# Kernel tuning notes

Hardware: AMD Instinct MI355X
Metric: run time of the kernel (lower is better)

The kernel has to match this reference:

```python
import jax, jax.numpy as jnp
import numpy as np

B, N, C = 2048, 4096, 1024
UNITS, RANK = 4096, 512


def _orth(key, shape):
    a = jax.random.normal(key, shape, dtype=jnp.float32)
    q, r = jnp.linalg.qr(a if shape[0] >= shape[1] else a.T)
    q = q * jnp.sign(jnp.diagonal(r))[None, :]
    return q if shape[0] >= shape[1] else q.T


def setup_inputs() -> dict:
    key = jax.random.key(0)
    k1, k2, k3, k4, k5, k6 = jax.random.split(key, 6)
    inputs = jax.random.normal(k1, (B, N), dtype=jnp.float32)
    context = jax.random.normal(k2, (B, C), dtype=jnp.float32)
    U = _orth(k3, (N, RANK))
    V = _orth(k4, (UNITS, RANK))
    W = _orth(k5, (C, RANK))
    # SingularValueInitializer stand-in: positive values scaled like glorot singular values
    S = jnp.abs(jax.random.normal(k6, (RANK,), dtype=jnp.float32)) * jnp.sqrt(2.0 / (N + UNITS))
    bias = jnp.zeros((UNITS,), dtype=jnp.float32)
    return {"inputs": inputs, "context": context, "U": U, "S": S, "V": V, "W": W, "bias": bias}


def reference(inputs, context, U, S, V, W, bias):
    # s_b = S + context @ W  -> per-batch singular values [B, R]
    s = S[None, :] + context @ W
    # Original: kernel_b = U diag(s_b) V^T; out_b = x_b @ kernel_b.
    # Associativity: out = ((x @ U) * s) @ V^T  -- identical math, no [B,N,M] intermediate.
    xu = inputs @ U                      # [B, R]
    out = (xu * s) @ V.T                 # [B, UNITS]
    out = out + bias[None, :]
    return jax.nn.relu(out)
```

## Files before the change

kernel.cpp:

```cpp
#include <hip/hip_runtime.h>
#include <hip/hip_bf16.h>

typedef __attribute__((ext_vector_type(8))) __bf16 bf16x8;
typedef __attribute__((ext_vector_type(4))) float f32x4;
typedef __attribute__((ext_vector_type(8))) unsigned short ushort8;
typedef __attribute__((ext_vector_type(4))) unsigned short ushort4v;

__device__ __forceinline__ unsigned short f2bf(float f) {
  unsigned u = __builtin_bit_cast(unsigned, f);
  u += 0x7FFFu + ((u >> 16) & 1u);
  return (unsigned short)(u >> 16);
}

__device__ __forceinline__ void gload_lds16(const void* g, void* l) {
  __builtin_amdgcn_global_load_lds(
      (const __attribute__((address_space(1))) void*)g,
      (__attribute__((address_space(3))) void*)l, 16, 0, 0);
}

__device__ __forceinline__ void barrier_fence() {
  __builtin_amdgcn_s_barrier();
  asm volatile("" ::: "memory");
}

template <int N>
__device__ __forceinline__ void waitvm() {
  if constexpr (N == 0)      asm volatile("s_waitcnt vmcnt(0)" ::: "memory");
  else if constexpr (N == 8) asm volatile("s_waitcnt vmcnt(8)" ::: "memory");
}

__global__ __launch_bounds__(256) void prep_kernel(
    const float* __restrict__ U, unsigned short* __restrict__ Ut,
    const float* __restrict__ W, unsigned short* __restrict__ Wt,
    const float* __restrict__ V, unsigned short* __restrict__ Vb) {
  __shared__ float tile[32][33];
  const int b = blockIdx.x;
  const int tid = threadIdx.x;
  if (b < 2560) {
    const float* src;
    unsigned short* dst;
    int rows, cols, bx, by;
    if (b < 2048) {
      src = U; dst = Ut; rows = 4096; cols = 512;
      bx = (b & 15) * 32; by = (b >> 4) * 32;
    } else {
      int bb = b - 2048;
      src = W; dst = Wt; rows = 1024; cols = 512;
      bx = (bb & 15) * 32; by = (bb >> 4) * 32;
    }
    const int tx = tid & 31, ty = tid >> 5;
    for (int i = ty; i < 32; i += 8)
      tile[i][tx] = src[(size_t)(by + i) * cols + bx + tx];
    __syncthreads();
    for (int i = ty; i < 32; i += 8)
      dst[(size_t)(bx + i) * rows + by + tx] = f2bf(tile[tx][i]);
  } else {
    const size_t i = (size_t)(b - 2560) * 256 + tid;
    const float4* s4 = reinterpret_cast<const float4*>(V) + 2 * i;
    float4 a = s4[0], c = s4[1];
    ushort8 o;
    o[0] = f2bf(a.x); o[1] = f2bf(a.y); o[2] = f2bf(a.z); o[3] = f2bf(a.w);
    o[4] = f2bf(c.x); o[5] = f2bf(c.y); o[6] = f2bf(c.z); o[7] = f2bf(c.w);
    *(reinterpret_cast<ushort8*>(Vb) + i) = o;
  }
}

template <int FM, int FN, int EPI, int DEPTH, bool COLMAP>
__device__ __forceinline__ void gemm_core(
    const unsigned short* __restrict__ A, const unsigned short* __restrict__ Bt,
    int N, int lda, int kchunk, const float* __restrict__ e0,
    float* __restrict__ outf, int nwg, int bid) {
  constexpr int BM = 32 * FM, BN = 32 * FN, BK = 64;
  constexpr int AI = FM, BI = FN;
  constexpr int ISS = AI + BI;
  __shared__ unsigned short lds[DEPTH][(BM + BN) * BK];

  const int tid = threadIdx.x;
  const int wid = tid >> 6;
  const int lane = tid & 63;
  const int wr = wid >> 1, wc = wid & 1;

  const int swz = (bid & 7) * (nwg >> 3) + (bid >> 3);
  const int nbn = N / BN;
  int brow, bcol;
  if constexpr (COLMAP) {
    const int nbm = nwg / nbn;
    brow = (swz % nbm) * BM;
    bcol = (swz / nbm) * BN;
  } else {
    brow = (swz / nbn) * BM;
    bcol = (swz % nbn) * BN;
  }

  f32x4 zero = {0.f, 0.f, 0.f, 0.f};
  f32x4 acc[FM][FN];
#pragma unroll
  for (int m = 0; m < FM; ++m)
#pragma unroll
    for (int n = 0; n < FN; ++n) acc[m][n] = zero;

  const int lr = lane >> 3;
  const int swzc = ((lane & 7) ^ lr) * 8;
  const unsigned short* Agh = A + (size_t)(brow + wid * (BM / 4) + lr) * lda + swzc;
  const unsigned short* Bgh = Bt + (size_t)(bcol + wid * (BN / 4) + lr) * lda + swzc;

  const int frow = lane & 15;
  const int fhi = lane >> 4;

  const int nsteps = kchunk / BK;

  auto stage = [&](int b, int kofs) {
    unsigned short* AsW = lds[b] + wid * (BM / 4) * 64;
#pragma unroll
    for (int i = 0; i < AI; ++i)
      gload_lds16(Agh + kofs + (size_t)(8 * i) * lda, AsW + i * 512);
    unsigned short* BsW = lds[b] + BM * BK + wid * (BN / 4) * 64;
#pragma unroll
    for (int i = 0; i < BI; ++i)
      gload_lds16(Bgh + kofs + (size_t)(8 * i) * lda, BsW + i * 512);
  };

  auto compute = [&](int cur) {
    const unsigned short* As = lds[cur];
    const unsigned short* Bs = lds[cur] + BM * BK;
#pragma unroll
    for (int ks = 0; ks < 2; ++ks) {
      bf16x8 af[FM], bg[FN];
#pragma unroll
      for (int m = 0; m < FM; ++m) {
        int row = wr * FM * 16 + m * 16 + frow;
        int pc = (ks * 4 + fhi) ^ (row & 7);
        af[m] = *reinterpret_cast<const bf16x8*>(As + row * 64 + pc * 8);
      }
#pragma unroll
      for (int n = 0; n < FN; ++n) {
        int row = wc * FN * 16 + n * 16 + frow;
        int pc = (ks * 4 + fhi) ^ (row & 7);
        bg[n] = *reinterpret_cast<const bf16x8*>(Bs + row * 64 + pc * 8);
      }
#pragma unroll
      for (int m = 0; m < FM; ++m)
#pragma unroll
        for (int n = 0; n < FN; ++n)
          acc[m][n] = __builtin_amdgcn_mfma_f32_16x16x32_bf16(af[m], bg[n],
                                                              acc[m][n], 0, 0, 0);
    }
  };

#pragma unroll
  for (int d = 0; d < DEPTH; ++d) stage(d, d * BK);

  int cur = 0;
  for (int t = 0; t < nsteps; ++t) {
    const int ahead = nsteps - 1 - t;
    if (ahead >= DEPTH - 1)
      waitvm<(DEPTH - 1) * ISS>();
    else
      waitvm<0>();
    barrier_fence();
    compute(cur);
    if (t + 1 < nsteps) {
      asm volatile("s_waitcnt lgkmcnt(0)" ::: "memory");
      barrier_fence();
      if (t + DEPTH < nsteps) stage(cur, (t + DEPTH) * BK);
    }
    cur = (cur + 1 == DEPTH) ? 0 : cur + 1;
  }

#pragma unroll
  for (int m = 0; m < FM; ++m) {
    int gr0 = brow + wr * FM * 16 + m * 16 + fhi * 4;
#pragma unroll
    for (int n = 0; n < FN; ++n) {
      int gc = bcol + wc * FN * 16 + n * 16 + frow;
#pragma unroll
      for (int j = 0; j < 4; ++j) {
        size_t idx = (size_t)(gr0 + j) * N + gc;
        float v = acc[m][n][j];
        if constexpr (EPI == 2) {
          v += e0[gc];
          outf[idx] = v > 0.f ? v : 0.f;
        } else {
          outf[idx] = v;
        }
      }
    }
  }
}

__device__ __forceinline__ void gemm_core_f32a(
    const float* __restrict__ A, const unsigned short* __restrict__ Bt,
    int lda, const float* __restrict__ e0,
    float* __restrict__ outf, int nwg, int bid) {
  constexpr int N = 512;
  constexpr int BM = 128, BN = 128, BK = 64;
  constexpr int kchunk = 1024;
  __shared__ unsigned short lds[2][(BM + BN) * BK];

  const int tid = threadIdx.x;
  const int wid = tid >> 6;
  const int lane = tid & 63;
  const int wr = wid >> 1, wc = wid & 1;

  const int swz = (bid & 7) * (nwg >> 3) + (bid >> 3);
  const int nbn = N / BN;
  const int brow = (swz / nbn) * BM;
  const int bcol = (swz % nbn) * BN;

  f32x4 zero = {0.f, 0.f, 0.f, 0.f};
  f32x4 acc[4][4];
#pragma unroll
  for (int m = 0; m < 4; ++m)
#pragma unroll
    for (int n = 0; n < 4; ++n) acc[m][n] = zero;

  const int lr = lane >> 3;
  const int lc = lane & 7;
  const int swzc = (lc ^ lr) * 8;
  const float* Agf = A + (size_t)(brow + wid * 32 + lr) * lda + swzc;
  const unsigned short* Bgh = Bt + (size_t)(bcol + wid * 32 + lr) * lda + swzc;

  const int frow = lane & 15;
  const int fhi = lane >> 4;

  const int nsteps = kchunk / BK;

  float4 areg[4][2];
  auto aload = [&](int kofs) {
#pragma unroll
    for (int i = 0; i < 4; ++i) {
      const float* s = Agf + kofs + (size_t)(8 * i) * lda;
      areg[i][0] = *reinterpret_cast<const float4*>(s);
      areg[i][1] = *reinterpret_cast<const float4*>(s + 4);
    }
  };
  auto awrite = [&](int b) {
    unsigned short* AsW = lds[b] + wid * 2048 + lane * 8;
#pragma unroll
    for (int i = 0; i < 4; ++i) {
      float4 x = areg[i][0], y = areg[i][1];
      ushort8 o;
      o[0] = f2bf(x.x); o[1] = f2bf(x.y); o[2] = f2bf(x.z); o[3] = f2bf(x.w);
      o[4] = f2bf(y.x); o[5] = f2bf(y.y); o[6] = f2bf(y.z); o[7] = f2bf(y.w);
      *reinterpret_cast<ushort8*>(AsW + i * 512) = o;
    }
  };
  auto bload = [&](int b, int kofs) {
    unsigned short* BsW = lds[b] + BM * BK + wid * 2048;
#pragma unroll
    for (int i = 0; i < 4; ++i)
      gload_lds16(Bgh + kofs + (size_t)(8 * i) * lda, BsW + i * 512);
  };

  auto compute = [&](int cur) {
    const unsigned short* As = lds[cur];
    const unsigned short* Bs = lds[cur] + BM * BK;
#pragma unroll
    for (int ks = 0; ks < 2; ++ks) {
      bf16x8 af[4], bg[4];
#pragma unroll
      for (int m = 0; m < 4; ++m) {
        int row = wr * 64 + m * 16 + frow;
        int pc = (ks * 4 + fhi) ^ (row & 7);
        af[m] = *reinterpret_cast<const bf16x8*>(As + row * 64 + pc * 8);
      }
#pragma unroll
      for (int n = 0; n < 4; ++n) {
        int row = wc * 64 + n * 16 + frow;
        int pc = (ks * 4 + fhi) ^ (row & 7);
        bg[n] = *reinterpret_cast<const bf16x8*>(Bs + row * 64 + pc * 8);
      }
#pragma unroll
      for (int m = 0; m < 4; ++m)
#pragma unroll
        for (int n = 0; n < 4; ++n)
          acc[m][n] = __builtin_amdgcn_mfma_f32_16x16x32_bf16(af[m], bg[n],
                                                              acc[m][n], 0, 0, 0);
    }
  };

  aload(0);
  bload(0, 0);
  waitvm<0>();
  awrite(0);
  aload(BK);
  asm volatile("s_waitcnt lgkmcnt(0)" ::: "memory");
  barrier_fence();

  for (int t = 0; t < nsteps; ++t) {
    const int cur = t & 1;
    if (t + 1 < nsteps) bload(cur ^ 1, (t + 1) * BK);
    compute(cur);
    if (t + 1 < nsteps) {
      waitvm<0>();
      awrite(cur ^ 1);
      if (t + 2 < nsteps) aload((t + 2) * BK);
      asm volatile("s_waitcnt lgkmcnt(0)" ::: "memory");
      barrier_fence();
    }
  }

#pragma unroll
  for (int m = 0; m < 4; ++m) {
    int gr0 = brow + wr * 64 + m * 16 + fhi * 4;
#pragma unroll
    for (int n = 0; n < 4; ++n) {
      int gc = bcol + wc * 64 + n * 16 + frow;
#pragma unroll
      for (int j = 0; j < 4; ++j) {
        float v = acc[m][n][j];
        if (e0) v += e0[gc];
        outf[(size_t)(gr0 + j) * N + gc] = v;
      }
    }
  }
}

__global__ __launch_bounds__(256) void gemm01_kernel(
    const float* __restrict__ inp, const unsigned short* __restrict__ Ut,
    const float* __restrict__ ctx, const unsigned short* __restrict__ Wt,
    const float* __restrict__ S, float* __restrict__ sbuf,
    float* __restrict__ p1) {
  const int bid = (int)blockIdx.x;
  constexpr size_t MN = (size_t)2048 * 512;
  const float* A;
  const unsigned short* Bt;
  int lda, nwg, lbid;
  const float* e0;
  float* outp;
  if (bid < 256) {
    const int split = bid >> 6;
    A = inp + (size_t)split * 1024;
    Bt = Ut + (size_t)split * 1024;
    lda = 4096; e0 = nullptr; outp = p1 + split * MN; nwg = 64; lbid = bid & 63;
  } else {
    A = ctx; Bt = Wt; lda = 1024; e0 = S; outp = sbuf; nwg = 64; lbid = bid - 256;
  }
  gemm_core_f32a(A, Bt, lda, e0, outp, nwg, lbid);
}

__global__ __launch_bounds__(256) void gemm2_kernel(
    const unsigned short* __restrict__ xus, const unsigned short* __restrict__ Vb,
    const float* __restrict__ bias, float* __restrict__ out) {
  gemm_core<4, 4, 2, 2, true>(xus, Vb, 4096, 512, 512, bias, out, 512,
                              (int)blockIdx.x);
}

__global__ void reduce_mul_kernel(const float* __restrict__ p1,
                                  const float* __restrict__ sbuf,
                                  unsigned short* __restrict__ xus, int MN) {
  int i = blockIdx.x * blockDim.x + threadIdx.x;
  size_t base = (size_t)i * 4;
  if (base >= (size_t)MN) return;
  float4 a = *reinterpret_cast<const float4*>(p1 + base);
  float4 b = *reinterpret_cast<const float4*>(p1 + (size_t)MN + base);
  float4 c = *reinterpret_cast<const float4*>(p1 + 2 * (size_t)MN + base);
  float4 d = *reinterpret_cast<const float4*>(p1 + 3 * (size_t)MN + base);
  float4 s = *reinterpret_cast<const float4*>(sbuf + base);
  float4 xu;
  xu.x = (a.x + b.x) + (c.x + d.x);
  xu.y = (a.y + b.y) + (c.y + d.y);
  xu.z = (a.z + b.z) + (c.z + d.z);
  xu.w = (a.w + b.w) + (c.w + d.w);
  ushort4v o;
  o[0] = f2bf(xu.x * s.x);
  o[1] = f2bf(xu.y * s.y);
  o[2] = f2bf(xu.z * s.z);
  o[3] = f2bf(xu.w * s.w);
  *reinterpret_cast<ushort4v*>(xus + base) = o;
}

extern "C" void kernel_launch(void* const* d_in, const int* in_sizes, int n_in,
                              void* d_out, int out_size, void* d_ws, size_t ws_size,
                              hipStream_t stream) {
  constexpr int Bm = 2048, Nn = 4096, Cc = 1024, UU = 4096, RR = 512;
  const float* inputs  = (const float*)d_in[0];
  const float* context = (const float*)d_in[1];
  const float* U       = (const float*)d_in[2];
  const float* S       = (const float*)d_in[3];
  const float* V       = (const float*)d_in[4];
  const float* W       = (const float*)d_in[5];
  const float* bias    = (const float*)d_in[6];
  float* out = (float*)d_out;

  char* p = (char*)d_ws;
  unsigned short* Ut   = (unsigned short*)p; p += (size_t)RR * Nn * 2;
  unsigned short* Wt   = (unsigned short*)p; p += (size_t)RR * Cc * 2;
  unsigned short* Vb   = (unsigned short*)p; p += (size_t)UU * RR * 2;
  float*          sbuf = (float*)p;          p += (size_t)Bm * RR * 4;
  float*          p1   = (float*)p;          p += (size_t)4 * Bm * RR * 4;
  unsigned short* xus  = (unsigned short*)p; p += (size_t)Bm * RR * 2;

  prep_kernel<<<3584, 256, 0, stream>>>(U, Ut, W, Wt, V, Vb);

  gemm01_kernel<<<320, 256, 0, stream>>>(inputs, Ut, context, Wt, S, sbuf, p1);

  reduce_mul_kernel<<<Bm * RR / 4 / 256, 256, 0, stream>>>(p1, sbuf, xus, Bm * RR);

  gemm2_kernel<<<512, 256, 0, stream>>>(xus, Vb, bias, out);
}
```

Measured before the change: 62.04 us.

## Store split-K partials in bf16 and split context GEMM to balance workgroups

The split-K partial sums of inputs@U and the context@W product are now written as bf16 instead of fp32, roughly halving partial-buffer traffic in both the GEMM epilogue and the reduce kernel. The context GEMM is also split into two K-chunks of 512, giving 384 workgroups all doing equal 512/1024-sized K work rather than 64 blocks doing a full 1024-K chunk. The S vector add moves into the reduce kernel, which now handles 8 elements per thread. Rounding the partials to bf16 before summation adds precision loss.

```diff
diff --git a/kernel.cpp b/kernel.cpp
--- a/kernel.cpp
+++ b/kernel.cpp
@@ -4,12 +4,15 @@
 typedef __attribute__((ext_vector_type(8))) __bf16 bf16x8;
 typedef __attribute__((ext_vector_type(4))) float f32x4;
 typedef __attribute__((ext_vector_type(8))) unsigned short ushort8;
-typedef __attribute__((ext_vector_type(4))) unsigned short ushort4v;
 
 __device__ __forceinline__ unsigned short f2bf(float f) {
   unsigned u = __builtin_bit_cast(unsigned, f);
   u += 0x7FFFu + ((u >> 16) & 1u);
   return (unsigned short)(u >> 16);
+}
+
+__device__ __forceinline__ float bf2f(unsigned short h) {
+  return __builtin_bit_cast(float, (unsigned)h << 16);
 }
 
 __device__ __forceinline__ void gload_lds16(const void* g, void* l) {
@@ -190,11 +193,9 @@
 
 __device__ __forceinline__ void gemm_core_f32a(
     const float* __restrict__ A, const unsigned short* __restrict__ Bt,
-    int lda, const float* __restrict__ e0,
-    float* __restrict__ outf, int nwg, int bid) {
+    int lda, int kchunk, unsigned short* __restrict__ outb, int nwg, int bid) {
   constexpr int N = 512;
   constexpr int BM = 128, BN = 128, BK = 64;
-  constexpr int kchunk = 1024;
   __shared__ unsigned short lds[2][(BM + BN) * BK];
 
   const int tid = threadIdx.x;
@@ -307,11 +308,8 @@
     for (int n = 0; n < 4; ++n) {
       int gc = bcol + wc * 64 + n * 16 + frow;
 #pragma unroll
-      for (int j = 0; j < 4; ++j) {
-        float v = acc[m][n][j];
-        if (e0) v += e0[gc];
-        outf[(size_t)(gr0 + j) * N + gc] = v;
-      }
+      for (int j = 0; j < 4; ++j)
+        outb[(size_t)(gr0 + j) * N + gc] = f2bf(acc[m][n][j]);
     }
   }
 }
@@ -319,24 +317,26 @@
 __global__ __launch_bounds__(256) void gemm01_kernel(
     const float* __restrict__ inp, const unsigned short* __restrict__ Ut,
     const float* __restrict__ ctx, const unsigned short* __restrict__ Wt,
-    const float* __restrict__ S, float* __restrict__ sbuf,
-    float* __restrict__ p1) {
+    unsigned short* __restrict__ p0b, unsigned short* __restrict__ p1b) {
   const int bid = (int)blockIdx.x;
   constexpr size_t MN = (size_t)2048 * 512;
   const float* A;
   const unsigned short* Bt;
-  int lda, nwg, lbid;
-  const float* e0;
-  float* outp;
+  int lda, kchunk, lbid;
+  unsigned short* outp;
   if (bid < 256) {
     const int split = bid >> 6;
     A = inp + (size_t)split * 1024;
     Bt = Ut + (size_t)split * 1024;
-    lda = 4096; e0 = nullptr; outp = p1 + split * MN; nwg = 64; lbid = bid & 63;
+    lda = 4096; kchunk = 1024; outp = p1b + split * MN; lbid = bid & 63;
   } else {
-    A = ctx; Bt = Wt; lda = 1024; e0 = S; outp = sbuf; nwg = 64; lbid = bid - 256;
-  }
-  gemm_core_f32a(A, Bt, lda, e0, outp, nwg, lbid);
+    const int sb = bid - 256;
+    const int split = sb >> 6;
+    A = ctx + (size_t)split * 512;
+    Bt = Wt + (size_t)split * 512;
+    lda = 1024; kchunk = 512; outp = p0b + split * MN; lbid = sb & 63;
+  }
+  gemm_core_f32a(A, Bt, lda, kchunk, outp, 64, lbid);
 }
 
 __global__ __launch_bounds__(256) void gemm2_kernel(
@@ -346,28 +346,30 @@
                               (int)blockIdx.x);
 }
 
-__global__ void reduce_mul_kernel(const float* __restrict__ p1,
-                                  const float* __restrict__ sbuf,
+__global__ void reduce_mul_kernel(const unsigned short* __restrict__ p1,
+                                  const unsigned short* __restrict__ p0,
+                                  const float* __restrict__ Svec,
                                   unsigned short* __restrict__ xus, int MN) {
   int i = blockIdx.x * blockDim.x + threadIdx.x;
-  size_t base = (size_t)i * 4;
+  size_t base = (size_t)i * 8;
   if (base >= (size_t)MN) return;
-  float4 a = *reinterpret_cast<const float4*>(p1 + base);
-  float4 b = *reinterpret_cast<const float4*>(p1 + (size_t)MN + base);
-  float4 c = *reinterpret_cast<const float4*>(p1 + 2 * (size_t)MN + base);
-  float4 d = *reinterpret_cast<const float4*>(p1 + 3 * (size_t)MN + base);
-  float4 s = *reinterpret_cast<const float4*>(sbuf + base);
-  float4 xu;
-  xu.x = (a.x + b.x) + (c.x + d.x);
-  xu.y = (a.y + b.y) + (c.y + d.y);
-  xu.z = (a.z + b.z) + (c.z + d.z);
-  xu.w = (a.w + b.w) + (c.w + d.w);
-  ushort4v o;
-  o[0] = f2bf(xu.x * s.x);
-  o[1] = f2bf(xu.y * s.y);
-  o[2] = f2bf(xu.z * s.z);
-  o[3] = f2bf(xu.w * s.w);
-  *reinterpret_cast<ushort4v*>(xus + base) = o;
+  float xu[8] = {0.f, 0.f, 0.f, 0.f, 0.f, 0.f, 0.f, 0.f};
+#pragma unroll
+  for (int k = 0; k < 4; ++k) {
+    ushort8 a = *reinterpret_cast<const ushort8*>(p1 + (size_t)k * MN + base);
+#pragma unroll
+    for (int j = 0; j < 8; ++j) xu[j] += bf2f(a[j]);
+  }
+  ushort8 s0 = *reinterpret_cast<const ushort8*>(p0 + base);
+  ushort8 s1 = *reinterpret_cast<const ushort8*>(p0 + (size_t)MN + base);
+  const float* sv = Svec + (base & 511);
+  ushort8 o;
+#pragma unroll
+  for (int j = 0; j < 8; ++j) {
+    float s = bf2f(s0[j]) + bf2f(s1[j]) + sv[j];
+    o[j] = f2bf(xu[j] * s);
+  }
+  *reinterpret_cast<ushort8*>(xus + base) = o;
 }
 
 extern "C" void kernel_launch(void* const* d_in, const int* in_sizes, int n_in,
@@ -387,15 +389,15 @@
   unsigned short* Ut   = (unsigned short*)p; p += (size_t)RR * Nn * 2;
   unsigned short* Wt   = (unsigned short*)p; p += (size_t)RR * Cc * 2;
   unsigned short* Vb   = (unsigned short*)p; p += (size_t)UU * RR * 2;
-  float*          sbuf = (float*)p;          p += (size_t)Bm * RR * 4;
-  float*          p1   = (float*)p;          p += (size_t)4 * Bm * RR * 4;
+  unsigned short* p0b  = (unsigned short*)p; p += (size_t)2 * Bm * RR * 2;
+  unsigned short* p1b  = (unsigned short*)p; p += (size_t)4 * Bm * RR * 2;
   unsigned short* xus  = (unsigned short*)p; p += (size_t)Bm * RR * 2;
 
   prep_kernel<<<3584, 256, 0, stream>>>(U, Ut, W, Wt, V, Vb);
 
-  gemm01_kernel<<<320, 256, 0, stream>>>(inputs, Ut, context, Wt, S, sbuf, p1);
-
-  reduce_mul_kernel<<<Bm * RR / 4 / 256, 256, 0, stream>>>(p1, sbuf, xus, Bm * RR);
+  gemm01_kernel<<<384, 256, 0, stream>>>(inputs, Ut, context, Wt, p0b, p1b);
+
+  reduce_mul_kernel<<<Bm * RR / 8 / 256, 256, 0, stream>>>(p1b, p0b, S, xus, Bm * RR);
 
   gemm2_kernel<<<512, 256, 0, stream>>>(xus, Vb, bias, out);
 }
```

After: 50.53 us (median of 3 runs). 1.23x faster.
